# Optimization experiments

Measured on AMD Instinct MI355X. Metric: run time of the kernel, lower is better.

The kernel has to match this reference:

```python
import jax, jax.numpy as jnp
import numpy as np

N, IN_DIM, H1, H2, Z1, Z2, Z3 = 8192, 1024, 512, 256, 64, 64, 64
Z = Z1 + Z2 + Z3

def _xavier(key, shape):
    fan_out, fan_in = shape
    lim = jnp.sqrt(6.0 / (fan_in + fan_out))
    return jax.random.uniform(key, shape, jnp.float32, -lim, lim)

def setup_inputs() -> dict:
    key = jax.random.key(0)
    ks = jax.random.split(key, 12)
    # sparse-ish row-normalized adjacency (dense storage, matches adj.mm on dense tensor)
    a = jax.random.uniform(ks[0], (N, N), jnp.float32)
    a = jnp.where(a > 0.996, a, 0.0)
    a = a + jnp.eye(N, dtype=jnp.float32)
    adj = a / jnp.sum(a, axis=1, keepdims=True)
    x = jax.random.normal(ks[1], (N, IN_DIM), jnp.float32)
    return {
        "adj": adj,
        "x": x,
        "W1": _xavier(ks[2], (H1, IN_DIM)),
        "W2": _xavier(ks[3], (H2, H1)),
        "Wm1": _xavier(ks[4], (Z1, H2)),
        "Wm2": _xavier(ks[5], (Z2, H2)),
        "Wm3": _xavier(ks[6], (Z3, H2)),
        "Wt": _xavier(ks[7], (Z, Z)),
        "bt": jnp.zeros((Z,), jnp.float32),
    }

def _gconv(adj, x, W, act=None):
    h = adj @ (x @ W.T)  # linear then aggregate; dropout is identity in eval
    return act(h) if act is not None else h

def reference(adj, x, W1, W2, Wm1, Wm2, Wm3, Wt, bt):
    x1 = _gconv(adj, x, W1, jax.nn.relu)            # [N, H1]
    x2 = _gconv(adj, x1, W2, jax.nn.relu)           # [N, H2]
    # six heads share x2 and adj; eval-mode reparameterize returns the means
    m1 = _gconv(adj, x2, Wm1)
    m2 = _gconv(adj, x2, Wm2)
    m3 = _gconv(adj, x2, Wm3)
    z = jnp.concatenate([m1, m2, m3], axis=1)       # [N, Z]
    trans_z = jax.nn.leaky_relu(z @ Wt.T + bt, 0.1) # dropout identity in eval
    pred = z @ trans_z.T                            # [N, N]
    return pred, jax.nn.sigmoid(x1), jax.nn.sigmoid(x2), z
```

## Files before the change

kernel.cpp:

```cpp
#include <hip/hip_runtime.h>
#include <hip/hip_bf16.h>
#include <math.h>

#define NN 8192
#define CAP 256

typedef __attribute__((ext_vector_type(8))) short short8;
typedef __attribute__((ext_vector_type(16))) float f32x16;

__global__ __launch_bounds__(256) void build_csr(
    const float* __restrict__ adj, unsigned short* __restrict__ cols,
    float* __restrict__ vals, int* __restrict__ cnt)
{
    const int row = blockIdx.x;
    const int tid = threadIdx.x;
    __shared__ int c;
    if (tid == 0) c = 0;
    __syncthreads();
    const float4* arow = (const float4*)(adj + (size_t)row * NN);
    for (int i = tid; i < NN / 4; i += 256) {
        const float4 v = arow[i];
        const int base = i * 4;
        if (v.x != 0.f) { int p = atomicAdd(&c, 1); if (p < CAP) { cols[(size_t)row*CAP+p] = (unsigned short)(base+0); vals[(size_t)row*CAP+p] = v.x; } }
        if (v.y != 0.f) { int p = atomicAdd(&c, 1); if (p < CAP) { cols[(size_t)row*CAP+p] = (unsigned short)(base+1); vals[(size_t)row*CAP+p] = v.y; } }
        if (v.z != 0.f) { int p = atomicAdd(&c, 1); if (p < CAP) { cols[(size_t)row*CAP+p] = (unsigned short)(base+2); vals[(size_t)row*CAP+p] = v.z; } }
        if (v.w != 0.f) { int p = atomicAdd(&c, 1); if (p < CAP) { cols[(size_t)row*CAP+p] = (unsigned short)(base+3); vals[(size_t)row*CAP+p] = v.w; } }
    }
    __syncthreads();
    if (tid == 0) cnt[row] = min(c, CAP);
}

template <int COLS, int RELU, int WRITE_SIG>
__global__ void spmm_kernel(
    const unsigned short* __restrict__ cols, const float* __restrict__ vals,
    const int* __restrict__ cnt, const float* __restrict__ H,
    float* __restrict__ out, float* __restrict__ sig_out)
{
    const int row = blockIdx.x;
    const int tid = threadIdx.x;
    __shared__ unsigned short lc[CAP];
    __shared__ float lv[CAP];
    const int n = cnt[row];
    for (int i = tid; i < n; i += COLS) {
        lc[i] = cols[(size_t)row * CAP + i];
        lv[i] = vals[(size_t)row * CAP + i];
    }
    __syncthreads();
    float acc = 0.f;
    int k = 0;
    for (; k + 4 <= n; k += 4) {
        const float a0 = lv[k+0] * H[(size_t)lc[k+0] * COLS + tid];
        const float a1 = lv[k+1] * H[(size_t)lc[k+1] * COLS + tid];
        const float a2 = lv[k+2] * H[(size_t)lc[k+2] * COLS + tid];
        const float a3 = lv[k+3] * H[(size_t)lc[k+3] * COLS + tid];
        acc += (a0 + a1) + (a2 + a3);
    }
    for (; k < n; ++k) acc += lv[k] * H[(size_t)lc[k] * COLS + tid];
    if (RELU) acc = fmaxf(acc, 0.f);
    out[(size_t)row * COLS + tid] = acc;
    if (WRITE_SIG) sig_out[(size_t)row * COLS + tid] = 1.f / (1.f + expf(-acc));
}

static __device__ __forceinline__ unsigned short f2bf(float f) {
    __hip_bfloat16 h = __float2bfloat16(f);
    return *reinterpret_cast<unsigned short*>(&h);
}
static __device__ __forceinline__ float bf2f(unsigned short u) {
    __hip_bfloat16 h = *reinterpret_cast<__hip_bfloat16*>(&u);
    return __bfloat162float(h);
}

__global__ __launch_bounds__(256) void pack_hilo(
    const float* __restrict__ in, unsigned short* __restrict__ hi,
    unsigned short* __restrict__ lo, int n4)
{
    for (int idx = blockIdx.x * 256 + threadIdx.x; idx < n4; idx += gridDim.x * 256) {
        const float4 v = ((const float4*)in)[idx];
        float f[4] = {v.x, v.y, v.z, v.w};
        ushort4 h, l;
        unsigned short* hp = (unsigned short*)&h;
        unsigned short* lp = (unsigned short*)&l;
        #pragma unroll
        for (int j = 0; j < 4; ++j) {
            const unsigned short hb = f2bf(f[j]);
            hp[j] = hb;
            lp[j] = f2bf(f[j] - bf2f(hb));
        }
        ((ushort4*)hi)[idx] = h;
        ((ushort4*)lo)[idx] = l;
    }
}

template <int ACT>
__global__ __launch_bounds__(256) void gemm3_bt(
    const unsigned short* __restrict__ Ahi, const unsigned short* __restrict__ Alo,
    const unsigned short* __restrict__ Bhi, const unsigned short* __restrict__ Blo,
    float* __restrict__ C, const float* __restrict__ bias,
    int K, int Nb, int ldC)
{
    __shared__ __align__(16) unsigned short As[128 * 64];
    __shared__ __align__(16) unsigned short Bs[128 * 64];
    const int bm = blockIdx.x * 128;
    const int bn = blockIdx.y * 128;
    const int tid = threadIdx.x;
    const int lane = tid & 63;
    const int wave = tid >> 6;
    const int wr = wave >> 1, wc = wave & 1;

    f32x16 acc[2][2] = {};

    for (int seg = 0; seg < 3; ++seg) {
        const unsigned short* Aseg = (seg == 1) ? Alo : Ahi;
        const unsigned short* Bseg = (seg == 2) ? Blo : Bhi;
        for (int kt = 0; kt < K; kt += 64) {
            #pragma unroll
            for (int call = 0; call < 4; ++call) {
                const int c = call * 256 + tid;
                const int row = c >> 3;
                const int slot = (c & 7) ^ (row & 7);
                const unsigned short* g = Aseg + (size_t)(bm + row) * K + kt + slot * 8;
                __builtin_amdgcn_global_load_lds(
                    (const __attribute__((address_space(1))) unsigned int*)g,
                    (__attribute__((address_space(3))) unsigned int*)&As[c * 8], 16, 0, 0);
            }
            #pragma unroll
            for (int call = 0; call < 4; ++call) {
                const int c = call * 256 + tid;
                const int row = c >> 3;
                const int slot = (c & 7) ^ (row & 7);
                int rg = bn + row; rg = rg < Nb ? rg : Nb - 1;
                const unsigned short* g = Bseg + (size_t)rg * K + kt + slot * 8;
                __builtin_amdgcn_global_load_lds(
                    (const __attribute__((address_space(1))) unsigned int*)g,
                    (__attribute__((address_space(3))) unsigned int*)&Bs[c * 8], 16, 0, 0);
            }
            __syncthreads();
            #pragma unroll
            for (int ks = 0; ks < 4; ++ks) {
                const int q = ks * 2 + (lane >> 5);
                short8 a[2], b[2];
                #pragma unroll
                for (int m = 0; m < 2; ++m) {
                    const int row = wr * 64 + m * 32 + (lane & 31);
                    const int s = q ^ (row & 7);
                    a[m] = *(const short8*)&As[row * 64 + s * 8];
                }
                #pragma unroll
                for (int n = 0; n < 2; ++n) {
                    const int row = wc * 64 + n * 32 + (lane & 31);
                    const int s = q ^ (row & 7);
                    b[n] = *(const short8*)&Bs[row * 64 + s * 8];
                }
                #pragma unroll
                for (int m = 0; m < 2; ++m)
                    #pragma unroll
                    for (int n = 0; n < 2; ++n)
                        acc[m][n] = __builtin_amdgcn_mfma_f32_32x32x16_bf16(
                            a[m], b[n], acc[m][n], 0, 0, 0);
            }
            __syncthreads();
        }
    }
    const int hi = lane >> 5;
    #pragma unroll
    for (int m = 0; m < 2; ++m) {
        #pragma unroll
        for (int n = 0; n < 2; ++n) {
            const int col = bn + wc * 64 + n * 32 + (lane & 31);
            if (col < Nb) {
                #pragma unroll
                for (int r = 0; r < 16; ++r) {
                    const int rl = (r & 3) + 8 * (r >> 2) + 4 * hi;
                    const size_t row = bm + wr * 64 + m * 32 + rl;
                    float v = acc[m][n][r];
                    if (ACT == 1) { v += bias[col]; v = v > 0.f ? v : 0.1f * v; }
                    C[row * (size_t)ldC + col] = v;
                }
            }
        }
    }
}

template <int ACT>
__global__ __launch_bounds__(256) void gemm_abt(
    const float* __restrict__ A, const float* __restrict__ B,
    float* __restrict__ C, const float* __restrict__ bias,
    int K, int ldC)
{
    __shared__ float As[16][132];
    __shared__ float Bs[16][68];
    const int bm = blockIdx.x * 128;
    const int bn = blockIdx.y * 64;
    const int tid = threadIdx.x;
    const int ty = tid >> 4;
    const int tx = tid & 15;
    float acc[8][4] = {};
    const float* Ab = A + (size_t)bm * K;
    const float* Bb = B + (size_t)bn * K;
    for (int kt = 0; kt < K; kt += 16) {
        #pragma unroll
        for (int j = 0; j < 2; ++j) {
            const int i = tid * 2 + j;
            const int row = i >> 2, kq = i & 3;
            const float4 v = *(const float4*)(Ab + (size_t)row * K + kt + kq * 4);
            As[kq*4+0][row] = v.x; As[kq*4+1][row] = v.y;
            As[kq*4+2][row] = v.z; As[kq*4+3][row] = v.w;
        }
        {
            const int row = tid >> 2, kq = tid & 3;
            const float4 v = *(const float4*)(Bb + (size_t)row * K + kt + kq * 4);
            Bs[kq*4+0][row] = v.x; Bs[kq*4+1][row] = v.y;
            Bs[kq*4+2][row] = v.z; Bs[kq*4+3][row] = v.w;
        }
        __syncthreads();
        #pragma unroll
        for (int kk = 0; kk < 16; ++kk) {
            float a[8], b[4];
            #pragma unroll
            for (int i2 = 0; i2 < 8; ++i2) a[i2] = As[kk][ty*8 + i2];
            #pragma unroll
            for (int j2 = 0; j2 < 4; ++j2) b[j2] = Bs[kk][tx*4 + j2];
            #pragma unroll
            for (int i2 = 0; i2 < 8; ++i2)
                #pragma unroll
                for (int j2 = 0; j2 < 4; ++j2)
                    acc[i2][j2] = fmaf(a[i2], b[j2], acc[i2][j2]);
        }
        __syncthreads();
    }
    #pragma unroll
    for (int i2 = 0; i2 < 8; ++i2) {
        const size_t r = bm + ty*8 + i2;
        #pragma unroll
        for (int j2 = 0; j2 < 4; ++j2) {
            const int cidx = bn + tx*4 + j2;
            float v = acc[i2][j2];
            if (ACT == 1) { v += bias[cidx]; v = v > 0.f ? v : 0.1f * v; }
            C[r * (size_t)ldC + cidx] = v;
        }
    }
}

extern "C" void kernel_launch(void* const* d_in, const int* in_sizes, int n_in,
                              void* d_out, int out_size, void* d_ws, size_t ws_size,
                              hipStream_t stream)
{
    const float* adj = (const float*)d_in[0];
    const float* x   = (const float*)d_in[1];
    const float* W1  = (const float*)d_in[2];
    const float* W2  = (const float*)d_in[3];
    const float* Wm1 = (const float*)d_in[4];
    const float* Wm2 = (const float*)d_in[5];
    const float* Wm3 = (const float*)d_in[6];
    const float* Wt  = (const float*)d_in[7];
    const float* bt  = (const float*)d_in[8];
    float* out = (float*)d_out;

    float* pred = out;
    float* sig1 = out + 67108864;
    float* sig2 = sig1 + 4194304;
    float* z    = sig2 + 2097152;

    char* w = (char*)d_ws;
    float* F  = (float*)w;              w += (size_t)8192*512*4;
    float* G  = (float*)w;              w += (size_t)8192*512*4;
    unsigned short* Xhi = (unsigned short*)w; w += (size_t)8192*1024*2;
    unsigned short* Xlo = (unsigned short*)w; w += (size_t)8192*1024*2;
    unsigned short* Whi = (unsigned short*)w; w += (size_t)512*1024*2;
    unsigned short* Wlo = (unsigned short*)w; w += (size_t)512*1024*2;
    unsigned short* Zhi = (unsigned short*)w; w += (size_t)8192*192*2;
    unsigned short* Zlo = (unsigned short*)w; w += (size_t)8192*192*2;
    unsigned short* Thi = (unsigned short*)w; w += (size_t)8192*192*2;
    unsigned short* Tlo = (unsigned short*)w; w += (size_t)8192*192*2;
    float* vals = (float*)w;            w += (size_t)NN*CAP*4;
    unsigned short* cols = (unsigned short*)w; w += (size_t)NN*CAP*2;
    int* cnt = (int*)w;                 w += (size_t)NN*4;
    const size_t need = (size_t)(w - (char*)d_ws);

    if (ws_size < need) {
        float* bufA = (float*)d_ws;
        float* bufB = bufA + 4194304;
        float* fvals = bufB + 4194304;
        unsigned short* fcols = (unsigned short*)(fvals + (size_t)NN * CAP);
        int* fcnt = (int*)(fcols + (size_t)NN * CAP);
        build_csr<<<NN, 256, 0, stream>>>(adj, fcols, fvals, fcnt);
        gemm_abt<0><<<dim3(64, 8), 256, 0, stream>>>(x, W1, bufA, nullptr, 1024, 512);
        spmm_kernel<512, 1, 1><<<NN, 512, 0, stream>>>(fcols, fvals, fcnt, bufA, bufB, sig1);
        gemm_abt<0><<<dim3(64, 4), 256, 0, stream>>>(bufB, W2, bufA, nullptr, 512, 256);
        spmm_kernel<256, 1, 1><<<NN, 256, 0, stream>>>(fcols, fvals, fcnt, bufA, bufB, sig2);
        gemm_abt<0><<<dim3(64, 1), 256, 0, stream>>>(bufB, Wm1, bufA +   0, nullptr, 256, 192);
        gemm_abt<0><<<dim3(64, 1), 256, 0, stream>>>(bufB, Wm2, bufA +  64, nullptr, 256, 192);
        gemm_abt<0><<<dim3(64, 1), 256, 0, stream>>>(bufB, Wm3, bufA + 128, nullptr, 256, 192);
        spmm_kernel<192, 0, 0><<<NN, 192, 0, stream>>>(fcols, fvals, fcnt, bufA, z, nullptr);
        gemm_abt<1><<<dim3(64, 3), 256, 0, stream>>>(z, Wt, bufB, bt, 192, 192);
        gemm_abt<0><<<dim3(64, 128), 256, 0, stream>>>(z, bufB, pred, nullptr, 192, 8192);
        return;
    }

    build_csr<<<NN, 256, 0, stream>>>(adj, cols, vals, cnt);

    pack_hilo<<<2048, 256, 0, stream>>>(x,  Xhi, Xlo, 8192*1024/4);
    pack_hilo<<<512,  256, 0, stream>>>(W1, Whi, Wlo, 512*1024/4);
    gemm3_bt<0><<<dim3(64, 4), 256, 0, stream>>>(Xhi, Xlo, Whi, Wlo, F, nullptr, 1024, 512, 512);
    spmm_kernel<512, 1, 1><<<NN, 512, 0, stream>>>(cols, vals, cnt, F, G, sig1);

    pack_hilo<<<2048, 256, 0, stream>>>(G,  Xhi, Xlo, 8192*512/4);
    pack_hilo<<<128,  256, 0, stream>>>(W2, Whi, Wlo, 256*512/4);
    gemm3_bt<0><<<dim3(64, 2), 256, 0, stream>>>(Xhi, Xlo, Whi, Wlo, F, nullptr, 512, 256, 256);
    spmm_kernel<256, 1, 1><<<NN, 256, 0, stream>>>(cols, vals, cnt, F, G, sig2);

    pack_hilo<<<2048, 256, 0, stream>>>(G,   Xhi, Xlo, 8192*256/4);
    pack_hilo<<<16,   256, 0, stream>>>(Wm1, Whi,            Wlo,            64*256/4);
    pack_hilo<<<16,   256, 0, stream>>>(Wm2, Whi +  64*256,  Wlo +  64*256,  64*256/4);
    pack_hilo<<<16,   256, 0, stream>>>(Wm3, Whi + 128*256,  Wlo + 128*256,  64*256/4);
    gemm3_bt<0><<<dim3(64, 2), 256, 0, stream>>>(Xhi, Xlo, Whi, Wlo, F, nullptr, 256, 192, 192);
    spmm_kernel<192, 0, 0><<<NN, 192, 0, stream>>>(cols, vals, cnt, F, z, nullptr);

    pack_hilo<<<1536, 256, 0, stream>>>(z,  Zhi, Zlo, 8192*192/4);
    pack_hilo<<<36,   256, 0, stream>>>(Wt, Whi, Wlo, 192*192/4);
    gemm3_bt<1><<<dim3(64, 2), 256, 0, stream>>>(Zhi, Zlo, Whi, Wlo, F, bt, 192, 192, 192);
    pack_hilo<<<1536, 256, 0, stream>>>(F, Thi, Tlo, 8192*192/4);

    gemm3_bt<0><<<dim3(64, 64), 256, 0, stream>>>(Zhi, Zlo, Thi, Tlo, pred, nullptr, 192, 8192, 8192);
}
```

Before: 819.4 us.

## Fuse hi/lo bf16 packing into SpMM and GEMM epilogues, retune GEMM tiles

The SpMM kernels now write bf16 hi/lo split outputs directly, and the Wt GEMM epilogue emits the packed trans_z. This removes the separate pack_hilo passes over the activations and the fp32 intermediate G buffer. The GEMM is templated on block and warp tile sizes, using smaller tiles for the skinny GEMMs (more blocks) and a 256x128 tile for the large pred GEMM. Larger tiles raise register pressure and lower occupancy, and uncoalesced 2-byte stores from the epilogues may cost some bandwidth.

```diff
diff --git a/kernel.cpp b/kernel.cpp
--- a/kernel.cpp
+++ b/kernel.cpp
@@ -7,6 +7,15 @@
 
 typedef __attribute__((ext_vector_type(8))) short short8;
 typedef __attribute__((ext_vector_type(16))) float f32x16;
+
+static __device__ __forceinline__ unsigned short f2bf(float f) {
+    __hip_bfloat16 h = __float2bfloat16(f);
+    return *reinterpret_cast<unsigned short*>(&h);
+}
+static __device__ __forceinline__ float bf2f(unsigned short u) {
+    __hip_bfloat16 h = *reinterpret_cast<__hip_bfloat16*>(&u);
+    return __bfloat162float(h);
+}
 
 __global__ __launch_bounds__(256) void build_csr(
     const float* __restrict__ adj, unsigned short* __restrict__ cols,
@@ -30,11 +39,12 @@
     if (tid == 0) cnt[row] = min(c, CAP);
 }
 
-template <int COLS, int RELU, int WRITE_SIG>
+template <int COLS, int RELU, int WSIG, int WOUT, int WHILO>
 __global__ void spmm_kernel(
     const unsigned short* __restrict__ cols, const float* __restrict__ vals,
     const int* __restrict__ cnt, const float* __restrict__ H,
-    float* __restrict__ out, float* __restrict__ sig_out)
+    float* __restrict__ out, float* __restrict__ sig_out,
+    unsigned short* __restrict__ hi, unsigned short* __restrict__ lo)
 {
     const int row = blockIdx.x;
     const int tid = threadIdx.x;
@@ -57,17 +67,14 @@
     }
     for (; k < n; ++k) acc += lv[k] * H[(size_t)lc[k] * COLS + tid];
     if (RELU) acc = fmaxf(acc, 0.f);
-    out[(size_t)row * COLS + tid] = acc;
-    if (WRITE_SIG) sig_out[(size_t)row * COLS + tid] = 1.f / (1.f + expf(-acc));
-}
-
-static __device__ __forceinline__ unsigned short f2bf(float f) {
-    __hip_bfloat16 h = __float2bfloat16(f);
-    return *reinterpret_cast<unsigned short*>(&h);
-}
-static __device__ __forceinline__ float bf2f(unsigned short u) {
-    __hip_bfloat16 h = *reinterpret_cast<__hip_bfloat16*>(&u);
-    return __bfloat162float(h);
+    const size_t idx = (size_t)row * COLS + tid;
+    if (WOUT) out[idx] = acc;
+    if (WSIG) sig_out[idx] = 1.f / (1.f + expf(-acc));
+    if (WHILO) {
+        const unsigned short h = f2bf(acc);
+        hi[idx] = h;
+        lo[idx] = f2bf(acc - bf2f(h));
+    }
 }
 
 __global__ __launch_bounds__(256) void pack_hilo(
@@ -91,30 +98,33 @@
     }
 }
 
-template <int ACT>
-__global__ __launch_bounds__(256) void gemm3_bt(
+template <int BM, int BN, int WM, int WN, int EPI>
+__global__ __launch_bounds__(256) void gemm3(
     const unsigned short* __restrict__ Ahi, const unsigned short* __restrict__ Alo,
     const unsigned short* __restrict__ Bhi, const unsigned short* __restrict__ Blo,
-    float* __restrict__ C, const float* __restrict__ bias,
+    float* __restrict__ C, unsigned short* __restrict__ Ohi,
+    unsigned short* __restrict__ Olo, const float* __restrict__ bias,
     int K, int Nb, int ldC)
 {
-    __shared__ __align__(16) unsigned short As[128 * 64];
-    __shared__ __align__(16) unsigned short Bs[128 * 64];
-    const int bm = blockIdx.x * 128;
-    const int bn = blockIdx.y * 128;
+    constexpr int FM = BM / (WM * 32);
+    constexpr int FN = BN / (WN * 32);
+    __shared__ __align__(16) unsigned short As[BM * 64];
+    __shared__ __align__(16) unsigned short Bs[BN * 64];
+    const int bm = blockIdx.x * BM;
+    const int bn = blockIdx.y * BN;
     const int tid = threadIdx.x;
     const int lane = tid & 63;
     const int wave = tid >> 6;
-    const int wr = wave >> 1, wc = wave & 1;
-
-    f32x16 acc[2][2] = {};
+    const int wr = wave / WN, wc = wave % WN;
+
+    f32x16 acc[FM][FN] = {};
 
     for (int seg = 0; seg < 3; ++seg) {
         const unsigned short* Aseg = (seg == 1) ? Alo : Ahi;
         const unsigned short* Bseg = (seg == 2) ? Blo : Bhi;
         for (int kt = 0; kt < K; kt += 64) {
             #pragma unroll
-            for (int call = 0; call < 4; ++call) {
+            for (int call = 0; call < BM / 32; ++call) {
                 const int c = call * 256 + tid;
                 const int row = c >> 3;
                 const int slot = (c & 7) ^ (row & 7);
@@ -124,7 +134,7 @@
                     (__attribute__((address_space(3))) unsigned int*)&As[c * 8], 16, 0, 0);
             }
             #pragma unroll
-            for (int call = 0; call < 4; ++call) {
+            for (int call = 0; call < BN / 32; ++call) {
                 const int c = call * 256 + tid;
                 const int row = c >> 3;
                 const int slot = (c & 7) ^ (row & 7);
@@ -138,43 +148,50 @@
             #pragma unroll
             for (int ks = 0; ks < 4; ++ks) {
                 const int q = ks * 2 + (lane >> 5);
-                short8 a[2], b[2];
-                #pragma unroll
-                for (int m = 0; m < 2; ++m) {
-                    const int row = wr * 64 + m * 32 + (lane & 31);
+                short8 a[FM], b[FN];
+                #pragma unroll
+                for (int m = 0; m < FM; ++m) {
+                    const int row = wr * (BM / WM) + m * 32 + (lane & 31);
                     const int s = q ^ (row & 7);
                     a[m] = *(const short8*)&As[row * 64 + s * 8];
                 }
                 #pragma unroll
-                for (int n = 0; n < 2; ++n) {
-                    const int row = wc * 64 + n * 32 + (lane & 31);
+                for (int n = 0; n < FN; ++n) {
+                    const int row = wc * (BN / WN) + n * 32 + (lane & 31);
                     const int s = q ^ (row & 7);
                     b[n] = *(const short8*)&Bs[row * 64 + s * 8];
                 }
                 #pragma unroll
-                for (int m = 0; m < 2; ++m)
+                for (int m = 0; m < FM; ++m)
                     #pragma unroll
-                    for (int n = 0; n < 2; ++n)
+                    for (int n = 0; n < FN; ++n)
                         acc[m][n] = __builtin_amdgcn_mfma_f32_32x32x16_bf16(
                             a[m], b[n], acc[m][n], 0, 0, 0);
             }
             __syncthreads();
         }
     }
-    const int hi = lane >> 5;
+    const int hl = lane >> 5;
     #pragma unroll
-    for (int m = 0; m < 2; ++m) {
-        #pragma unroll
-        for (int n = 0; n < 2; ++n) {
-            const int col = bn + wc * 64 + n * 32 + (lane & 31);
+    for (int m = 0; m < FM; ++m) {
+        #pragma unroll
+        for (int n = 0; n < FN; ++n) {
+            const int col = bn + wc * (BN / WN) + n * 32 + (lane & 31);
             if (col < Nb) {
                 #pragma unroll
                 for (int r = 0; r < 16; ++r) {
-                    const int rl = (r & 3) + 8 * (r >> 2) + 4 * hi;
-                    const size_t row = bm + wr * 64 + m * 32 + rl;
+                    const int rl = (r & 3) + 8 * (r >> 2) + 4 * hl;
+                    const size_t row = bm + wr * (BM / WM) + m * 32 + rl;
                     float v = acc[m][n][r];
-                    if (ACT == 1) { v += bias[col]; v = v > 0.f ? v : 0.1f * v; }
-                    C[row * (size_t)ldC + col] = v;
+                    if (EPI == 1) {
+                        v += bias[col];
+                        v = v > 0.f ? v : 0.1f * v;
+                        const unsigned short h = f2bf(v);
+                        Ohi[row * (size_t)ldC + col] = h;
+                        Olo[row * (size_t)ldC + col] = f2bf(v - bf2f(h));
+                    } else {
+                        C[row * (size_t)ldC + col] = v;
+                    }
                 }
             }
         }
@@ -262,19 +279,18 @@
     float* z    = sig2 + 2097152;
 
     char* w = (char*)d_ws;
-    float* F  = (float*)w;              w += (size_t)8192*512*4;
-    float* G  = (float*)w;              w += (size_t)8192*512*4;
-    unsigned short* Xhi = (unsigned short*)w; w += (size_t)8192*1024*2;
-    unsigned short* Xlo = (unsigned short*)w; w += (size_t)8192*1024*2;
-    unsigned short* Whi = (unsigned short*)w; w += (size_t)512*1024*2;
-    unsigned short* Wlo = (unsigned short*)w; w += (size_t)512*1024*2;
-    unsigned short* Zhi = (unsigned short*)w; w += (size_t)8192*192*2;
-    unsigned short* Zlo = (unsigned short*)w; w += (size_t)8192*192*2;
-    unsigned short* Thi = (unsigned short*)w; w += (size_t)8192*192*2;
-    unsigned short* Tlo = (unsigned short*)w; w += (size_t)8192*192*2;
-    float* vals = (float*)w;            w += (size_t)NN*CAP*4;
+    float* F  = (float*)w;                     w += (size_t)8192*512*4;
+    unsigned short* Xhi = (unsigned short*)w;  w += (size_t)8192*1024*2;
+    unsigned short* Xlo = (unsigned short*)w;  w += (size_t)8192*1024*2;
+    unsigned short* Whi = (unsigned short*)w;  w += (size_t)512*1024*2;
+    unsigned short* Wlo = (unsigned short*)w;  w += (size_t)512*1024*2;
+    unsigned short* Zhi = (unsigned short*)w;  w += (size_t)8192*192*2;
+    unsigned short* Zlo = (unsigned short*)w;  w += (size_t)8192*192*2;
+    unsigned short* Thi = (unsigned short*)w;  w += (size_t)8192*192*2;
+    unsigned short* Tlo = (unsigned short*)w;  w += (size_t)8192*192*2;
+    float* vals = (float*)w;                   w += (size_t)NN*CAP*4;
     unsigned short* cols = (unsigned short*)w; w += (size_t)NN*CAP*2;
-    int* cnt = (int*)w;                 w += (size_t)NN*4;
+    int* cnt = (int*)w;                        w += (size_t)NN*4;
     const size_t need = (size_t)(w - (char*)d_ws);
 
     if (ws_size < need) {
@@ -285,13 +301,13 @@
         int* fcnt = (int*)(fcols + (size_t)NN * CAP);
         build_csr<<<NN, 256, 0, stream>>>(adj, fcols, fvals, fcnt);
         gemm_abt<0><<<dim3(64, 8), 256, 0, stream>>>(x, W1, bufA, nullptr, 1024, 512);
-        spmm_kernel<512, 1, 1><<<NN, 512, 0, stream>>>(fcols, fvals, fcnt, bufA, bufB, sig1);
+        spmm_kernel<512, 1, 1, 1, 0><<<NN, 512, 0, stream>>>(fcols, fvals, fcnt, bufA, bufB, sig1, nullptr, nullptr);
         gemm_abt<0><<<dim3(64, 4), 256, 0, stream>>>(bufB, W2, bufA, nullptr, 512, 256);
-        spmm_kernel<256, 1, 1><<<NN, 256, 0, stream>>>(fcols, fvals, fcnt, bufA, bufB, sig2);
+        spmm_kernel<256, 1, 1, 1, 0><<<NN, 256, 0, stream>>>(fcols, fvals, fcnt, bufA, bufB, sig2, nullptr, nullptr);
         gemm_abt<0><<<dim3(64, 1), 256, 0, stream>>>(bufB, Wm1, bufA +   0, nullptr, 256, 192);
         gemm_abt<0><<<dim3(64, 1), 256, 0, stream>>>(bufB, Wm2, bufA +  64, nullptr, 256, 192);
         gemm_abt<0><<<dim3(64, 1), 256, 0, stream>>>(bufB, Wm3, bufA + 128, nullptr, 256, 192);
-        spmm_kernel<192, 0, 0><<<NN, 192, 0, stream>>>(fcols, fvals, fcnt, bufA, z, nullptr);
+        spmm_kernel<192, 0, 0, 1, 0><<<NN, 192, 0, stream>>>(fcols, fvals, fcnt, bufA, z, nullptr, nullptr, nullptr);
         gemm_abt<1><<<dim3(64, 3), 256, 0, stream>>>(z, Wt, bufB, bt, 192, 192);
         gemm_abt<0><<<dim3(64, 128), 256, 0, stream>>>(z, bufB, pred, nullptr, 192, 8192);
         return;
@@ -301,25 +317,29 @@
 
     pack_hilo<<<2048, 256, 0, stream>>>(x,  Xhi, Xlo, 8192*1024/4);
     pack_hilo<<<512,  256, 0, stream>>>(W1, Whi, Wlo, 512*1024/4);
-    gemm3_bt<0><<<dim3(64, 4), 256, 0, stream>>>(Xhi, Xlo, Whi, Wlo, F, nullptr, 1024, 512, 512);
-    spmm_kernel<512, 1, 1><<<NN, 512, 0, stream>>>(cols, vals, cnt, F, G, sig1);
-
-    pack_hilo<<<2048, 256, 0, stream>>>(G,  Xhi, Xlo, 8192*512/4);
-    pack_hilo<<<128,  256, 0, stream>>>(W2, Whi, Wlo, 256*512/4);
-    gemm3_bt<0><<<dim3(64, 2), 256, 0, stream>>>(Xhi, Xlo, Whi, Wlo, F, nullptr, 512, 256, 256);
-    spmm_kernel<256, 1, 1><<<NN, 256, 0, stream>>>(cols, vals, cnt, F, G, sig2);
-
-    pack_hilo<<<2048, 256, 0, stream>>>(G,   Xhi, Xlo, 8192*256/4);
-    pack_hilo<<<16,   256, 0, stream>>>(Wm1, Whi,            Wlo,            64*256/4);
-    pack_hilo<<<16,   256, 0, stream>>>(Wm2, Whi +  64*256,  Wlo +  64*256,  64*256/4);
-    pack_hilo<<<16,   256, 0, stream>>>(Wm3, Whi + 128*256,  Wlo + 128*256,  64*256/4);
-    gemm3_bt<0><<<dim3(64, 2), 256, 0, stream>>>(Xhi, Xlo, Whi, Wlo, F, nullptr, 256, 192, 192);
-    spmm_kernel<192, 0, 0><<<NN, 192, 0, stream>>>(cols, vals, cnt, F, z, nullptr);
-
-    pack_hilo<<<1536, 256, 0, stream>>>(z,  Zhi, Zlo, 8192*192/4);
-    pack_hilo<<<36,   256, 0, stream>>>(Wt, Whi, Wlo, 192*192/4);
-    gemm3_bt<1><<<dim3(64, 2), 256, 0, stream>>>(Zhi, Zlo, Whi, Wlo, F, bt, 192, 192, 192);
-    pack_hilo<<<1536, 256, 0, stream>>>(F, Thi, Tlo, 8192*192/4);
-
-    gemm3_bt<0><<<dim3(64, 64), 256, 0, stream>>>(Zhi, Zlo, Thi, Tlo, pred, nullptr, 192, 8192, 8192);
-}
+    gemm3<64, 128, 2, 2, 0><<<dim3(128, 4), 256, 0, stream>>>(
+        Xhi, Xlo, Whi, Wlo, F, nullptr, nullptr, nullptr, 1024, 512, 512);
+    spmm_kernel<512, 1, 1, 0, 1><<<NN, 512, 0, stream>>>(
+        cols, vals, cnt, F, nullptr, sig1, Xhi, Xlo);
+
+    pack_hilo<<<128, 256, 0, stream>>>(W2, Whi, Wlo, 256*512/4);
+    gemm3<64, 128, 2, 2, 0><<<dim3(128, 2), 256, 0, stream>>>(
+        Xhi, Xlo, Whi, Wlo, F, nullptr, nullptr, nullptr, 512, 256, 256);
+    spmm_kernel<256, 1, 1, 0, 1><<<NN, 256, 0, stream>>>(
+        cols, vals, cnt, F, nullptr, sig2, Xhi, Xlo);
+
+    pack_hilo<<<16, 256, 0, stream>>>(Wm1, Whi,           Wlo,           64*256/4);
+    pack_hilo<<<16, 256, 0, stream>>>(Wm2, Whi +  64*256, Wlo +  64*256, 64*256/4);
+    pack_hilo<<<16, 256, 0, stream>>>(Wm3, Whi + 128*256, Wlo + 128*256, 64*256/4);
+    gemm3<64, 64, 2, 2, 0><<<dim3(128, 3), 256, 0, stream>>>(
+        Xhi, Xlo, Whi, Wlo, F, nullptr, nullptr, nullptr, 256, 192, 192);
+    spmm_kernel<192, 0, 0, 1, 1><<<NN, 192, 0, stream>>>(
+        cols, vals, cnt, F, z, nullptr, Zhi, Zlo);
+
+    pack_hilo<<<36, 256, 0, stream>>>(Wt, Whi, Wlo, 192*192/4);
+    gemm3<64, 64, 2, 2, 1><<<dim3(128, 3), 256, 0, stream>>>(
+        Zhi, Zlo, Whi, Wlo, nullptr, Thi, Tlo, bt, 192, 192, 192);
+
+    gemm3<256, 128, 2, 2, 0><<<dim3(32, 64), 256, 0, stream>>>(
+        Zhi, Zlo, Thi, Tlo, pred, nullptr, nullptr, nullptr, 192, 8192, 8192);
+}
```

Result: no change. 828.5 us (+1.1%).
